# Performance work log

Measured on AMD Instinct MI355X. Metric: run time of the kernel, lower is better.

## Reference

```python
import jax, jax.numpy as jnp
import numpy as np

D_MODEL, D_FF, N_EXPERTS, TOP_K = 1024, 4096, 8, 2
B, S = 4, 1024
EPS = 1e-5

def setup_inputs() -> dict:
    key = jax.random.key(0)
    ks = jax.random.split(key, 8)
    sd = 1.0 / np.sqrt(D_MODEL)
    sf = 1.0 / np.sqrt(D_FF)
    return {
        "x": jax.random.normal(ks[0], (B, S, D_MODEL), dtype=jnp.float32),
        "mask": jnp.ones((B, S), dtype=bool),
        "Wg": jax.random.normal(ks[1], (D_MODEL, N_EXPERTS), dtype=jnp.float32) * sd,
        "W1": jax.random.normal(ks[2], (N_EXPERTS, D_MODEL, D_FF), dtype=jnp.float32) * sd,
        "b1": jnp.zeros((N_EXPERTS, D_FF), dtype=jnp.float32),
        "W2": jax.random.normal(ks[3], (N_EXPERTS, D_FF, D_MODEL), dtype=jnp.float32) * sf,
        "b2": jnp.zeros((N_EXPERTS, D_MODEL), dtype=jnp.float32),
        "gamma": jnp.ones((D_MODEL,), dtype=jnp.float32),
        "beta": jnp.zeros((D_MODEL,), dtype=jnp.float32),
    }

def _layernorm(x, gamma, beta):
    mu = jnp.mean(x, axis=-1, keepdims=True)
    var = jnp.mean(jnp.square(x - mu), axis=-1, keepdims=True)
    return (x - mu) * jax.lax.rsqrt(var + EPS) * gamma + beta

def reference(x, mask, Wg, W1, b1, W2, b2, gamma, beta):
    Bq, Sq, D = x.shape
    T = Bq * Sq
    xf = x.reshape(T, D)                       # [T, D]
    logits = xf @ Wg                           # [T, E]
    probs = jax.nn.softmax(logits, axis=-1)
    topv, topi = jax.lax.top_k(probs, TOP_K)   # [T, K]
    w = topv / jnp.sum(topv, axis=-1, keepdims=True)
    combine = jnp.zeros((T, N_EXPERTS), dtype=probs.dtype)
    combine = combine.at[jnp.arange(T)[:, None], topi].add(w)  # [T, E]
    # all-expert FFN (dense reference for grouped expert GEMMs)
    h = jax.nn.relu(jnp.einsum('td,edf->tef', xf, W1) + b1)    # [T, E, F]
    ye = jnp.einsum('tef,efd->ted', h, W2) + b2                # [T, E, D]
    y = jnp.einsum('te,ted->td', combine, ye)                  # [T, D]
    # load-balancing aux loss (Switch-style)
    frac_tokens = jnp.mean((combine > 0).astype(probs.dtype), axis=0)  # [E]
    frac_probs = jnp.mean(probs, axis=0)                                # [E]
    aux_loss = N_EXPERTS * jnp.sum(frac_tokens * frac_probs)
    out = _layernorm(x + y.reshape(Bq, Sq, D), gamma, beta)
    return out, aux_loss
```

## Files before the change

kernel.cpp:

```cpp
#include <hip/hip_runtime.h>
#include <cstdint>
#include <cstddef>


#define T_TOK 4096
#define DM 1024
#define DF 4096
#define NE 8
#define CAP 9216
#define MAXMT 72

typedef __bf16 bf16;
typedef __bf16 bf16x4 __attribute__((ext_vector_type(4)));
typedef __bf16 bf16x8 __attribute__((ext_vector_type(8)));
typedef float f32x4 __attribute__((ext_vector_type(4)));

struct Meta {
  int pad_off[NE + 1];
  int n_mtiles;
  int tile_e[80];
  int tile_m0[80];
};

__global__ __launch_bounds__(256) void router_kernel(
    const float* __restrict__ x, const float* __restrict__ Wg,
    int* __restrict__ topi, float* __restrict__ topw, float* __restrict__ probs) {
  int wave = threadIdx.x >> 6, lane = threadIdx.x & 63;
  int t = blockIdx.x * 4 + wave;
  const float* xr = x + (size_t)t * DM;
  float acc[NE];
#pragma unroll
  for (int e = 0; e < NE; e++) acc[e] = 0.f;
  for (int d0 = 0; d0 < DM; d0 += 64) {
    float xv = xr[d0 + lane];
    const float4* wrow = (const float4*)(Wg + (size_t)(d0 + lane) * NE);
    float4 w0 = wrow[0], w1 = wrow[1];
    acc[0] += xv * w0.x; acc[1] += xv * w0.y; acc[2] += xv * w0.z; acc[3] += xv * w0.w;
    acc[4] += xv * w1.x; acc[5] += xv * w1.y; acc[6] += xv * w1.z; acc[7] += xv * w1.w;
  }
#pragma unroll
  for (int off = 32; off >= 1; off >>= 1) {
#pragma unroll
    for (int e = 0; e < NE; e++) acc[e] += __shfl_xor(acc[e], off);
  }
  if (lane == 0) {
    float m = acc[0];
#pragma unroll
    for (int e = 1; e < NE; e++) m = fmaxf(m, acc[e]);
    float p[NE], s = 0.f;
#pragma unroll
    for (int e = 0; e < NE; e++) { p[e] = expf(acc[e] - m); s += p[e]; }
    float inv = 1.f / s;
#pragma unroll
    for (int e = 0; e < NE; e++) { p[e] *= inv; probs[t * NE + e] = p[e]; }
    int i1 = 0; float v1 = acc[0];
#pragma unroll
    for (int e = 1; e < NE; e++) if (acc[e] > v1) { v1 = acc[e]; i1 = e; }
    int i2 = -1; float v2 = -1e30f;
#pragma unroll
    for (int e = 0; e < NE; e++) if (e != i1 && acc[e] > v2) { v2 = acc[e]; i2 = e; }
    float sw = p[i1] + p[i2];
    topi[t * 2] = i1; topi[t * 2 + 1] = i2;
    topw[t * 2] = p[i1] / sw; topw[t * 2 + 1] = p[i2] / sw;
  }
}

__global__ __launch_bounds__(256) void prep_kernel(
    const int* __restrict__ topi, const float* __restrict__ probs,
    Meta* __restrict__ meta, float* __restrict__ aux_out) {
  __shared__ int scnt[NE];
  __shared__ float wps[4][NE];
  int tid = threadIdx.x, lane = tid & 63, wave = tid >> 6;
  if (tid < NE) scnt[tid] = 0;
  __syncthreads();
  for (int i = tid; i < T_TOK * 2; i += 256) atomicAdd(&scnt[topi[i]], 1);
  float lp[NE];
#pragma unroll
  for (int e = 0; e < NE; e++) lp[e] = 0.f;
  for (int tt = tid; tt < T_TOK; tt += 256) {
#pragma unroll
    for (int e = 0; e < NE; e++) lp[e] += probs[tt * NE + e];
  }
#pragma unroll
  for (int off = 32; off >= 1; off >>= 1) {
#pragma unroll
    for (int e = 0; e < NE; e++) lp[e] += __shfl_xor(lp[e], off);
  }
  if (lane == 0) {
#pragma unroll
    for (int e = 0; e < NE; e++) wps[wave][e] = lp[e];
  }
  __syncthreads();
  if (tid == 0) {
    float aux = 0.f;
    int nt = 0, po = 0;
    for (int e = 0; e < NE; e++) {
      float ps = wps[0][e] + wps[1][e] + wps[2][e] + wps[3][e];
      aux += (float)scnt[e] * ps;
      meta->pad_off[e] = po;
      int pc = (scnt[e] + 127) & ~127;
      for (int i = 0; i < pc / 128; i++) {
        meta->tile_e[nt] = e; meta->tile_m0[nt] = po + i * 128; nt++;
      }
      po += pc;
    }
    meta->pad_off[NE] = po;
    meta->n_mtiles = nt;
    aux_out[0] = aux * (8.f / ((float)T_TOK * (float)T_TOK));
  }
}

__global__ __launch_bounds__(64) void scatter_kernel(
    const int* __restrict__ topi, const float* __restrict__ topw,
    const Meta* __restrict__ meta,
    int* __restrict__ t_of, float* __restrict__ w_of, int* __restrict__ k_of) {
  int e = blockIdx.x, lane = threadIdx.x;
  int base = meta->pad_off[e];
  for (int c = 0; c < T_TOK * 2; c += 64) {
    int idx = c + lane;
    int sel = (topi[idx] == e) ? 1 : 0;
    unsigned long long mask = __ballot(sel);
    if (sel) {
      int rank = __popcll(mask & ((1ull << lane) - 1ull));
      int s = base + rank;
      t_of[s] = idx >> 1;
      k_of[s] = idx & 1;
      w_of[s] = topw[idx];
    }
    base += (int)__popcll(mask);
  }
}

__global__ __launch_bounds__(256) void gather_kernel(
    const float* __restrict__ x, const int* __restrict__ t_of,
    unsigned short* __restrict__ Xg_u) {
  int s = blockIdx.x;
  int t = t_of[s];
  if (t < 0) return;
  bf16* Xg = (bf16*)Xg_u;
  int i = threadIdx.x;
  float4 v = ((const float4*)(x + (size_t)t * DM))[i];
  bf16x4 o = {(bf16)v.x, (bf16)v.y, (bf16)v.z, (bf16)v.w};
  ((bf16x4*)(Xg + (size_t)s * DM))[i] = o;
}

__global__ __launch_bounds__(256) void transpose_kernel(
    const float* __restrict__ src, unsigned short* __restrict__ dst_u, int R, int C) {
  bf16* dst = (bf16*)dst_u;
  int e = blockIdx.z;
  int c0 = blockIdx.x * 64, r0 = blockIdx.y * 64;
  __shared__ float tile[64][69];
  const float* s = src + (size_t)e * R * C;
  int lr = threadIdx.x >> 4;
  int lc4 = (threadIdx.x & 15) * 4;
#pragma unroll
  for (int p = 0; p < 4; p++) {
    float4 v = *(const float4*)&s[(size_t)(r0 + p * 16 + lr) * C + c0 + lc4];
    tile[p * 16 + lr][lc4]     = v.x;
    tile[p * 16 + lr][lc4 + 1] = v.y;
    tile[p * 16 + lr][lc4 + 2] = v.z;
    tile[p * 16 + lr][lc4 + 3] = v.w;
  }
  __syncthreads();
  bf16* d = dst + (size_t)e * C * R;
#pragma unroll
  for (int s2 = 0; s2 < 2; s2++) {
    int q = threadIdx.x + 256 * s2;
    int c = q >> 3;
    int rs = (q & 7) * 8;
    bf16x8 o;
#pragma unroll
    for (int j = 0; j < 8; j++) o[j] = (bf16)tile[rs + j][c];
    *(bf16x8*)&d[(size_t)(c0 + c) * R + r0 + rs] = o;
  }
}

__device__ inline void gl_lds16(const void* g, void* l) {
  __builtin_amdgcn_global_load_lds(
      (const __attribute__((address_space(1))) unsigned int*)g,
      (__attribute__((address_space(3))) unsigned int*)l, 16, 0, 0);
}

template <int MODE>
__global__ __launch_bounds__(256) void gemm_kernel(
    const unsigned short* __restrict__ A_u, const unsigned short* __restrict__ Bt_u,
    const float* __restrict__ bias, const Meta* __restrict__ meta,
    int Ktot, int Ksp, int N,
    unsigned short* __restrict__ Hout_u,
    float* __restrict__ P0, float* __restrict__ P1,
    const int* __restrict__ t_of, const int* __restrict__ k_of,
    const float* __restrict__ w_of) {
  int id = blockIdx.x + gridDim.x * (blockIdx.y + gridDim.y * blockIdx.z);
  int xcd = id & 7;
  int rr = id >> 3;
  int chunk = gridDim.x >> 3;
  int bx = xcd * chunk + rr % chunk;
  int rest = rr / chunk;
  int n0 = (rest % gridDim.y) * 128;
  int bz = rest / gridDim.y;

  if (bx >= meta->n_mtiles) return;
  const bf16* A = (const bf16*)A_u;
  const bf16* Bt = (const bf16*)Bt_u;
  int e = meta->tile_e[bx];
  int m0 = meta->tile_m0[bx];
  int koff = bz * Ksp;
  const bf16* Be = Bt + (size_t)e * N * Ktot;

  __shared__ bf16 As[128 * 64];
  __shared__ bf16 Bs[128 * 64];

  int tid = threadIdx.x, lane = tid & 63, wave = tid >> 6;
  int wr = wave >> 1, wc = wave & 1;
  int srow = lane >> 3;
  int sgran = lane & 7;
  int gcol = (sgran ^ srow) * 8;

  const bf16* Ag = A + (size_t)(m0 + wave * 8 + srow) * Ktot + koff + gcol;
  const bf16* Bg = Be + (size_t)(n0 + wave * 8 + srow) * Ktot + koff + gcol;
  bf16* AsW = As + wave * 512;
  bf16* BsW = Bs + wave * 512;

  f32x4 acc[4][4];
#pragma unroll
  for (int i = 0; i < 4; i++)
#pragma unroll
    for (int j = 0; j < 4; j++) acc[i][j] = (f32x4){0.f, 0.f, 0.f, 0.f};

  int fr = lane & 15;
  int qh = lane >> 4;
  int swz = fr & 7;

  for (int k0 = 0; k0 < Ksp; k0 += 64) {
#pragma unroll
    for (int r = 0; r < 4; r++) {
      gl_lds16(Ag + (size_t)(r * 32) * Ktot + k0, AsW + r * 2048);
      gl_lds16(Bg + (size_t)(r * 32) * Ktot + k0, BsW + r * 2048);
    }
    __syncthreads();
#pragma unroll
    for (int kk = 0; kk < 64; kk += 32) {
      int col = (((kk >> 3) | qh) ^ swz) * 8;
      bf16x8 af[4], bfr[4];
#pragma unroll
      for (int i = 0; i < 4; i++)
        af[i] = *(const bf16x8*)&As[(wr * 64 + i * 16 + fr) * 64 + col];
#pragma unroll
      for (int j = 0; j < 4; j++)
        bfr[j] = *(const bf16x8*)&Bs[(wc * 64 + j * 16 + fr) * 64 + col];
#pragma unroll
      for (int i = 0; i < 4; i++)
#pragma unroll
        for (int j = 0; j < 4; j++)
          acc[i][j] = __builtin_amdgcn_mfma_f32_16x16x32_bf16(af[i], bfr[j], acc[i][j], 0, 0, 0);
    }
    __syncthreads();
  }

  int crow = (lane >> 4) * 4;
  int ccol = lane & 15;
  if (MODE == 1) {
    bf16* Hout = (bf16*)Hout_u;
#pragma unroll
    for (int i = 0; i < 4; i++) {
#pragma unroll
      for (int r = 0; r < 4; r++) {
        int slot = m0 + wr * 64 + i * 16 + crow + r;
        bf16* hrow = Hout + (size_t)slot * N;
#pragma unroll
        for (int j = 0; j < 4; j++) {
          int n = n0 + wc * 64 + j * 16 + ccol;
          float v = acc[i][j][r] + bias[e * N + n];
          hrow[n] = (bf16)fmaxf(v, 0.f);
        }
      }
    }
  } else {
    float* Pz = (bz == 0) ? P0 : P1;
    int addb = (bz == 0) ? 1 : 0;
#pragma unroll
    for (int i = 0; i < 4; i++) {
#pragma unroll
      for (int r = 0; r < 4; r++) {
        int slot = m0 + wr * 64 + i * 16 + crow + r;
        int t = t_of[slot];
        if (t < 0) continue;
        int ks = k_of[slot];
        float w = w_of[slot];
        float* yrow = Pz + ((size_t)ks * T_TOK + t) * DM;
#pragma unroll
        for (int j = 0; j < 4; j++) {
          int n = n0 + wc * 64 + j * 16 + ccol;
          float bv = addb ? bias[e * DM + n] : 0.f;
          yrow[n] = (acc[i][j][r] + bv) * w;
        }
      }
    }
  }
}

__global__ __launch_bounds__(256) void ln_kernel(
    const float* __restrict__ x,
    const float* __restrict__ P0, const float* __restrict__ P1,
    const float* __restrict__ gamma, const float* __restrict__ beta,
    float* __restrict__ out) {
  int t = blockIdx.x, tid = threadIdx.x, lane = tid & 63, wave = tid >> 6;
  size_t row = (size_t)t * DM;
  size_t kstride = (size_t)T_TOK * DM;
  float4 a  = ((const float4*)(x + row))[tid];
  float4 y0 = ((const float4*)(P0 + row))[tid];
  float4 y1 = ((const float4*)(P0 + kstride + row))[tid];
  float4 y2 = ((const float4*)(P1 + row))[tid];
  float4 y3 = ((const float4*)(P1 + kstride + row))[tid];
  float4 sv;
  sv.x = a.x + y0.x + y1.x + y2.x + y3.x;
  sv.y = a.y + y0.y + y1.y + y2.y + y3.y;
  sv.z = a.z + y0.z + y1.z + y2.z + y3.z;
  sv.w = a.w + y0.w + y1.w + y2.w + y3.w;
  float sum = sv.x + sv.y + sv.z + sv.w;
  float sq = sv.x * sv.x + sv.y * sv.y + sv.z * sv.z + sv.w * sv.w;
#pragma unroll
  for (int off = 32; off >= 1; off >>= 1) {
    sum += __shfl_xor(sum, off);
    sq += __shfl_xor(sq, off);
  }
  __shared__ float ls[4], lq[4], stats[2];
  if (lane == 0) { ls[wave] = sum; lq[wave] = sq; }
  __syncthreads();
  if (tid == 0) {
    float ts = ls[0] + ls[1] + ls[2] + ls[3];
    float tq = lq[0] + lq[1] + lq[2] + lq[3];
    float mu = ts * (1.f / DM);
    float var = tq * (1.f / DM) - mu * mu;
    stats[0] = mu;
    stats[1] = rsqrtf(var + 1e-5f);
  }
  __syncthreads();
  float mu = stats[0], rs = stats[1];
  float4 g = ((const float4*)gamma)[tid];
  float4 b = ((const float4*)beta)[tid];
  float4 o;
  o.x = (sv.x - mu) * rs * g.x + b.x;
  o.y = (sv.y - mu) * rs * g.y + b.y;
  o.z = (sv.z - mu) * rs * g.z + b.z;
  o.w = (sv.w - mu) * rs * g.w + b.w;
  ((float4*)(out + row))[tid] = o;
}

extern "C" void kernel_launch(void* const* d_in, const int* in_sizes, int n_in,
                              void* d_out, int out_size, void* d_ws, size_t ws_size,
                              hipStream_t stream) {
  const float* x     = (const float*)d_in[0];
  const float* Wg    = (const float*)d_in[2];
  const float* W1    = (const float*)d_in[3];
  const float* b1    = (const float*)d_in[4];
  const float* W2    = (const float*)d_in[5];
  const float* b2    = (const float*)d_in[6];
  const float* gamma = (const float*)d_in[7];
  const float* beta  = (const float*)d_in[8];
  float* out = (float*)d_out;

  char* ws = (char*)d_ws;
  size_t off = 0;
  auto alloc = [&](size_t bytes) -> void* {
    off = (off + 4095) & ~(size_t)4095;
    void* p = ws + off;
    off += bytes;
    return p;
  };
  Meta* meta   = (Meta*)alloc(sizeof(Meta));
  int* topi    = (int*)alloc((size_t)T_TOK * 2 * 4);
  float* topw  = (float*)alloc((size_t)T_TOK * 2 * 4);
  float* probs = (float*)alloc((size_t)T_TOK * NE * 4);
  int* t_of    = (int*)alloc((size_t)CAP * 4);
  int* k_of    = (int*)alloc((size_t)CAP * 4);
  float* w_of  = (float*)alloc((size_t)CAP * 4);
  size_t xg_bytes = (size_t)CAP * DM * 2;
  size_t p_bytes  = (size_t)2 * T_TOK * DM * 4;
  char* xg_region = (char*)alloc(xg_bytes > p_bytes ? xg_bytes : p_bytes);
  unsigned short* Xg = (unsigned short*)xg_region;
  float* Psp1        = (float*)xg_region;
  unsigned short* Hbuf = (unsigned short*)alloc((size_t)CAP * DF * 2);
  float* Psp0          = (float*)alloc(p_bytes);
  unsigned short* WT   = (unsigned short*)alloc((size_t)NE * DM * DF * 2);

  hipMemsetAsync(t_of, 0xFF, (size_t)CAP * 4, stream);

  router_kernel<<<dim3(T_TOK / 4), dim3(256), 0, stream>>>(x, Wg, topi, topw, probs);
  prep_kernel<<<dim3(1), dim3(256), 0, stream>>>(topi, probs, meta, out + (size_t)T_TOK * DM);
  scatter_kernel<<<dim3(NE), dim3(64), 0, stream>>>(topi, topw, meta, t_of, w_of, k_of);
  gather_kernel<<<dim3(CAP), dim3(256), 0, stream>>>(x, t_of, Xg);

  transpose_kernel<<<dim3(DF / 64, DM / 64, NE), dim3(256), 0, stream>>>(W1, WT, DM, DF);
  gemm_kernel<1><<<dim3(MAXMT, DF / 128, 1), dim3(256), 0, stream>>>(
      Xg, WT, b1, meta, DM, DM, DF, Hbuf, (float*)nullptr, (float*)nullptr,
      (const int*)nullptr, (const int*)nullptr, (const float*)nullptr);

  transpose_kernel<<<dim3(DM / 64, DF / 64, NE), dim3(256), 0, stream>>>(W2, WT, DF, DM);
  gemm_kernel<2><<<dim3(MAXMT, DM / 128, 2), dim3(256), 0, stream>>>(
      Hbuf, WT, b2, meta, DF, DF / 2, DM, (unsigned short*)nullptr, Psp0, Psp1,
      t_of, k_of, w_of);

  ln_kernel<<<dim3(T_TOK), dim3(256), 0, stream>>>(x, Psp0, Psp1, gamma, beta, out);
}
```

Baseline: 643.4 us.

## Fuse prep and scatter kernels and shrink GEMM K-tile to 32

Merges the routing-count prep kernel and the per-expert scatter into one 512-thread block. The block caches topi in shared memory and writes the -1 padding itself, which removes the memset and one launch. Separately, the grouped GEMM now stages a K-tile of 32 instead of 64, halving shared memory per block. This may raise occupancy but doubles the number of barrier-separated iterations and gives less MFMA work per sync.

```diff
diff --git a/kernel.cpp b/kernel.cpp
--- a/kernel.cpp
+++ b/kernel.cpp
@@ -65,19 +65,27 @@
   }
 }
 
-__global__ __launch_bounds__(256) void prep_kernel(
-    const int* __restrict__ topi, const float* __restrict__ probs,
-    Meta* __restrict__ meta, float* __restrict__ aux_out) {
+__global__ __launch_bounds__(512) void prep_scatter_kernel(
+    const int* __restrict__ topi, const float* __restrict__ topw,
+    const float* __restrict__ probs,
+    Meta* __restrict__ meta, float* __restrict__ aux_out,
+    int* __restrict__ t_of, float* __restrict__ w_of, int* __restrict__ k_of) {
+  __shared__ int stopi[T_TOK * 2];
   __shared__ int scnt[NE];
-  __shared__ float wps[4][NE];
+  __shared__ int spo[NE + 1];
+  __shared__ float wps[8][NE];
   int tid = threadIdx.x, lane = tid & 63, wave = tid >> 6;
   if (tid < NE) scnt[tid] = 0;
   __syncthreads();
-  for (int i = tid; i < T_TOK * 2; i += 256) atomicAdd(&scnt[topi[i]], 1);
+  for (int i = tid; i < T_TOK * 2; i += 512) {
+    int v = topi[i];
+    stopi[i] = v;
+    atomicAdd(&scnt[v], 1);
+  }
   float lp[NE];
 #pragma unroll
   for (int e = 0; e < NE; e++) lp[e] = 0.f;
-  for (int tt = tid; tt < T_TOK; tt += 256) {
+  for (int tt = tid; tt < T_TOK; tt += 512) {
 #pragma unroll
     for (int e = 0; e < NE; e++) lp[e] += probs[tt * NE + e];
   }
@@ -95,8 +103,10 @@
     float aux = 0.f;
     int nt = 0, po = 0;
     for (int e = 0; e < NE; e++) {
-      float ps = wps[0][e] + wps[1][e] + wps[2][e] + wps[3][e];
+      float ps = 0.f;
+      for (int w = 0; w < 8; w++) ps += wps[w][e];
       aux += (float)scnt[e] * ps;
+      spo[e] = po;
       meta->pad_off[e] = po;
       int pc = (scnt[e] + 127) & ~127;
       for (int i = 0; i < pc / 128; i++) {
@@ -104,21 +114,17 @@
       }
       po += pc;
     }
+    spo[NE] = po;
     meta->pad_off[NE] = po;
     meta->n_mtiles = nt;
     aux_out[0] = aux * (8.f / ((float)T_TOK * (float)T_TOK));
   }
-}
-
-__global__ __launch_bounds__(64) void scatter_kernel(
-    const int* __restrict__ topi, const float* __restrict__ topw,
-    const Meta* __restrict__ meta,
-    int* __restrict__ t_of, float* __restrict__ w_of, int* __restrict__ k_of) {
-  int e = blockIdx.x, lane = threadIdx.x;
-  int base = meta->pad_off[e];
+  __syncthreads();
+  int e = wave;
+  int base = spo[e];
   for (int c = 0; c < T_TOK * 2; c += 64) {
     int idx = c + lane;
-    int sel = (topi[idx] == e) ? 1 : 0;
+    int sel = (stopi[idx] == e) ? 1 : 0;
     unsigned long long mask = __ballot(sel);
     if (sel) {
       int rank = __popcll(mask & ((1ull << lane) - 1ull));
@@ -129,6 +135,8 @@
     }
     base += (int)__popcll(mask);
   }
+  for (int s = base + lane; s < spo[e + 1]; s += 64) t_of[s] = -1;
+  for (int s = spo[NE] + tid; s < CAP; s += 512) t_of[s] = -1;
 }
 
 __global__ __launch_bounds__(256) void gather_kernel(
@@ -207,19 +215,19 @@
   int koff = bz * Ksp;
   const bf16* Be = Bt + (size_t)e * N * Ktot;
 
-  __shared__ bf16 As[128 * 64];
-  __shared__ bf16 Bs[128 * 64];
+  __shared__ bf16 As[128 * 32];
+  __shared__ bf16 Bs[128 * 32];
 
   int tid = threadIdx.x, lane = tid & 63, wave = tid >> 6;
   int wr = wave >> 1, wc = wave & 1;
-  int srow = lane >> 3;
-  int sgran = lane & 7;
-  int gcol = (sgran ^ srow) * 8;
-
-  const bf16* Ag = A + (size_t)(m0 + wave * 8 + srow) * Ktot + koff + gcol;
-  const bf16* Bg = Be + (size_t)(n0 + wave * 8 + srow) * Ktot + koff + gcol;
-  bf16* AsW = As + wave * 512;
-  bf16* BsW = Bs + wave * 512;
+  int srow = lane >> 2;
+  int sgran = lane & 3;
+  int gcol = ((sgran ^ (srow & 3)) * 8);
+
+  const bf16* Ag = A + (size_t)(m0 + wave * 32 + srow) * Ktot + koff + gcol;
+  const bf16* Bg = Be + (size_t)(n0 + wave * 32 + srow) * Ktot + koff + gcol;
+  bf16* AsW = As + wave * 1024;
+  bf16* BsW = Bs + wave * 1024;
 
   f32x4 acc[4][4];
 #pragma unroll
@@ -228,32 +236,28 @@
     for (int j = 0; j < 4; j++) acc[i][j] = (f32x4){0.f, 0.f, 0.f, 0.f};
 
   int fr = lane & 15;
-  int qh = lane >> 4;
-  int swz = fr & 7;
-
-  for (int k0 = 0; k0 < Ksp; k0 += 64) {
-#pragma unroll
-    for (int r = 0; r < 4; r++) {
-      gl_lds16(Ag + (size_t)(r * 32) * Ktot + k0, AsW + r * 2048);
-      gl_lds16(Bg + (size_t)(r * 32) * Ktot + k0, BsW + r * 2048);
-    }
+  int q = lane >> 4;
+  int fcol = ((q ^ (fr & 3)) * 8);
+
+  const size_t rstep = (size_t)16 * Ktot;
+  for (int k0 = 0; k0 < Ksp; k0 += 32) {
+    gl_lds16(Ag + k0, AsW);
+    gl_lds16(Ag + rstep + k0, AsW + 512);
+    gl_lds16(Bg + k0, BsW);
+    gl_lds16(Bg + rstep + k0, BsW + 512);
     __syncthreads();
-#pragma unroll
-    for (int kk = 0; kk < 64; kk += 32) {
-      int col = (((kk >> 3) | qh) ^ swz) * 8;
-      bf16x8 af[4], bfr[4];
-#pragma unroll
-      for (int i = 0; i < 4; i++)
-        af[i] = *(const bf16x8*)&As[(wr * 64 + i * 16 + fr) * 64 + col];
+    bf16x8 af[4], bfr[4];
+#pragma unroll
+    for (int i = 0; i < 4; i++)
+      af[i] = *(const bf16x8*)&As[(wr * 64 + i * 16 + fr) * 32 + fcol];
+#pragma unroll
+    for (int j = 0; j < 4; j++)
+      bfr[j] = *(const bf16x8*)&Bs[(wc * 64 + j * 16 + fr) * 32 + fcol];
+#pragma unroll
+    for (int i = 0; i < 4; i++)
 #pragma unroll
       for (int j = 0; j < 4; j++)
-        bfr[j] = *(const bf16x8*)&Bs[(wc * 64 + j * 16 + fr) * 64 + col];
-#pragma unroll
-      for (int i = 0; i < 4; i++)
-#pragma unroll
-        for (int j = 0; j < 4; j++)
-          acc[i][j] = __builtin_amdgcn_mfma_f32_16x16x32_bf16(af[i], bfr[j], acc[i][j], 0, 0, 0);
-    }
+        acc[i][j] = __builtin_amdgcn_mfma_f32_16x16x32_bf16(af[i], bfr[j], acc[i][j], 0, 0, 0);
     __syncthreads();
   }
 
@@ -384,11 +388,9 @@
   float* Psp0          = (float*)alloc(p_bytes);
   unsigned short* WT   = (unsigned short*)alloc((size_t)NE * DM * DF * 2);
 
-  hipMemsetAsync(t_of, 0xFF, (size_t)CAP * 4, stream);
-
   router_kernel<<<dim3(T_TOK / 4), dim3(256), 0, stream>>>(x, Wg, topi, topw, probs);
-  prep_kernel<<<dim3(1), dim3(256), 0, stream>>>(topi, probs, meta, out + (size_t)T_TOK * DM);
-  scatter_kernel<<<dim3(NE), dim3(64), 0, stream>>>(topi, topw, meta, t_of, w_of, k_of);
+  prep_scatter_kernel<<<dim3(1), dim3(512), 0, stream>>>(
+      topi, topw, probs, meta, out + (size_t)T_TOK * DM, t_of, w_of, k_of);
   gather_kernel<<<dim3(CAP), dim3(256), 0, stream>>>(x, t_of, Xg);
 
   transpose_kernel<<<dim3(DF / 64, DM / 64, NE), dim3(256), 0, stream>>>(W1, WT, DM, DF);
```

Measured after the change: 644.6 us. No clear change (+0.2%).
